# Kernel optimization log

Hardware: AMD Instinct MI355X
Metric: run time of the kernel (lower is better)

The kernel has to match this reference:

```python
import math
import jax, jax.numpy as jnp
import numpy as np

H = 12   # num attention heads
DH = 64  # head dim
K = 2    # pooling kernel
ST = 2   # pooling stride


def _alibi_slopes(n):
    def pow2_slopes(n):
        start = 2 ** (-2 ** (-(math.log2(n) - 3)))
        return [start * (start ** i) for i in range(n)]
    if math.log2(n).is_integer():
        return pow2_slopes(n)
    c = 2 ** math.floor(math.log2(n))
    return pow2_slopes(c) + _alibi_slopes(2 * c)[0::2][: n - c]


def _alibi_bias(p, s):
    # [1, H, p, s]; -slope * |i - j|
    rel = np.abs(np.arange(s)[None, :] - np.arange(p)[:, None]).astype(np.float32)
    slopes = np.asarray(_alibi_slopes(H), dtype=np.float32)
    return jnp.asarray((-slopes[:, None, None] * rel[None])[None])


def masked_avg_pool(x, mask):
    # x: [b, S, d] float, mask: [b, S] bool
    b, S, d = x.shape
    pad = (K - S) if K > S else (S - K) % ST
    if pad:
        x = jnp.pad(x, ((0, 0), (0, pad), (0, 0)))
        mask = jnp.pad(mask, ((0, 0), (0, pad)))
    p = (S + pad - K) // ST + 1
    idx = jnp.arange(p)[:, None] * ST + jnp.arange(K)[None, :]  # [p, K]
    xb = x[:, idx]        # [b, p, K, d]
    mb = mask[:, idx]     # [b, p, K]
    norm = jnp.maximum(mb.sum(-1), 1).astype(x.dtype)  # [b, p]
    y = (xb * mb[..., None].astype(x.dtype)).sum(-2) / norm[..., None]
    return y, mb.any(-1)


def setup_inputs() -> dict:
    key = jax.random.key(0)
    k1, k2, k3, k4 = jax.random.split(key, 4)
    B, S, D = 64, 512, 768
    return {
        "hidden_states": jax.random.normal(k1, (B, S, D), dtype=jnp.float32),
        "attention_mask": jax.random.randint(k2, (B, S), 0, 2, dtype=jnp.int32),
        "Wqkv_w": jax.random.normal(k3, (D, 3 * D), dtype=jnp.float32) * 0.02,
        "Wqkv_b": jax.random.normal(k4, (3 * D,), dtype=jnp.float32) * 0.02,
    }


def reference(hidden_states, attention_mask, Wqkv_w, Wqkv_b):
    mask = attention_mask.astype(bool)                    # [b, s]
    b, s, _ = hidden_states.shape
    # fused QKV proj; repad() zeroes padded rows
    qkv = (hidden_states @ Wqkv_w + Wqkv_b) * mask[..., None].astype(hidden_states.dtype)
    q, k, v = jnp.split(qkv, 3, axis=-1)                  # each [b, s, H*DH]
    # masked avg pooling of queries (flattened heads, as in the module)
    q_pooled, new_mask = masked_avg_pool(q, mask)         # [b, p, H*DH], [b, p]
    p = q_pooled.shape[1]
    qh = q_pooled.reshape(b, p, H, DH).transpose(0, 2, 1, 3)  # [b, H, p, DH]
    kh = k.reshape(b, s, H, DH).transpose(0, 2, 1, 3)         # [b, H, s, DH]
    vh = v.reshape(b, s, H, DH).transpose(0, 2, 1, 3)
    # additive bias: 0 where both query and key valid, else -10000; plus ALiBi
    pair = new_mask[:, :, None] & mask[:, None, :]            # [b, p, s]
    bias = jnp.where(pair, 0.0, -10000.0)[:, None] + _alibi_bias(p, s)  # [b, H, p, s]
    scores = jnp.einsum("bhpd,bhsd->bhps", qh, kh) / math.sqrt(DH) + bias
    attn = jax.nn.softmax(scores, axis=-1)
    out = jnp.einsum("bhps,bhsd->bhpd", attn, vh)             # [b, H, p, DH]
    attn_output = out.transpose(0, 2, 1, 3).reshape(b, p, H * DH)
    nm = new_mask[..., None].astype(attn_output.dtype)
    attn_output = attn_output * nm        # emulate unpad(): zero invalid rows
    residual_query = q_pooled * nm
    return attn_output, new_mask, residual_query
```

## Files before the change

### kernel.cpp

```cpp
#include <hip/hip_runtime.h>
#include <cstdint>
#include <cstddef>

#define HH 12
#define DHD 64
#define BB 64
#define SS 512
#define DD 768
#define PP 256
#define N3 2304

typedef __attribute__((ext_vector_type(8))) short bf16x8_t;
typedef __attribute__((ext_vector_type(4))) float f32x4_t;

__constant__ float c_slopes[12] = {
  0.5f, 0.25f, 0.125f, 0.0625f, 0.03125f, 0.015625f, 0.0078125f, 0.00390625f,
  0.70710678118654752f, 0.35355339059327376f, 0.17677669529663688f, 0.08838834764831844f
};

__device__ __forceinline__ ushort f2bf(float f) {
  union { float f; unsigned u; } v; v.f = f;
  unsigned r = v.u + 0x7fffu + ((v.u >> 16) & 1u);
  return (ushort)(r >> 16);
}
__device__ __forceinline__ float bf2f(ushort u) {
  union { unsigned u; float f; } v; v.u = ((unsigned)u) << 16;
  return v.f;
}
__device__ __forceinline__ void gload_lds16(const ushort* g, ushort* l) {
  __builtin_amdgcn_global_load_lds(
      (const __attribute__((address_space(1))) void*)g,
      (__attribute__((address_space(3))) void*)l, 16, 0, 0);
}

__global__ __launch_bounds__(256) void prep_kernel(const float* __restrict__ in,
                                                   ushort* __restrict__ out,
                                                   const float* __restrict__ W,
                                                   ushort* __restrict__ Wt) {
  if (blockIdx.x < 24576) {
    int i = blockIdx.x * 256 + threadIdx.x;
    float4 v = ((const float4*)in)[i];
    ushort4 o;
    o.x = f2bf(v.x); o.y = f2bf(v.y); o.z = f2bf(v.z); o.w = f2bf(v.w);
    ((ushort4*)out)[i] = o;
  } else {
    __shared__ float tile[32][33];
    int tb = blockIdx.x - 24576;
    int n0 = (tb % 72) * 32, k0 = (tb / 72) * 32;
    int tx = threadIdx.x & 31, ty = threadIdx.x >> 5;
    for (int r = ty; r < 32; r += 8) tile[r][tx] = W[(size_t)(k0 + r) * N3 + n0 + tx];
    __syncthreads();
    for (int r = ty; r < 32; r += 8) Wt[(size_t)(n0 + r) * DD + k0 + tx] = f2bf(tile[tx][r]);
  }
}

__global__ __launch_bounds__(512, 2) void gemm_qkv_kernel(
    const ushort* __restrict__ A, const ushort* __restrict__ Wt,
    const float* __restrict__ bias, const int* __restrict__ mask,
    ushort* __restrict__ qkv) {
  __shared__ __align__(16) ushort As[2][16384];
  __shared__ __align__(16) ushort Bs[2][16384];
  const int wg = blockIdx.x;
  const int swz = (wg & 7) * 144 + (wg >> 3);
  const int bm = (swz / 9) * 256;
  const int bn = (swz % 9) * 256;
  const int tid = threadIdx.x;
  const int lane = tid & 63;
  const int wave = tid >> 6;
  const int wm = (wave >> 2) * 128;
  const int wn = (wave & 3) * 64;
  const int fr = lane & 15, quad = lane >> 4;
  const int xr = (fr & 7) << 3;
  const int q8 = quad * 8;

  const int rsub = tid >> 3;
  const int cg8 = ((tid & 7) ^ (rsub & 7)) * 8;
  const ushort* Ag = A  + (size_t)(bm + rsub) * DD + cg8;
  const ushort* Bg = Wt + (size_t)(bn + rsub) * DD + cg8;
  ushort* AsW = &As[0][0] + wave * 512;
  ushort* BsW = &Bs[0][0] + wave * 512;

  f32x4_t acc[8][4];
#pragma unroll
  for (int i = 0; i < 8; i++)
#pragma unroll
    for (int j = 0; j < 4; j++) acc[i][j] = (f32x4_t){0.f, 0.f, 0.f, 0.f};

#pragma unroll
  for (int l = 0; l < 4; l++) {
    gload_lds16(Ag + (size_t)l * 64 * DD,      AsW + l * 4096);
    gload_lds16(Bg + (size_t)l * 64 * DD,      BsW + l * 4096);
  }
#pragma unroll
  for (int l = 0; l < 4; l++) {
    gload_lds16(Ag + (size_t)l * 64 * DD + 64, AsW + 16384 + l * 4096);
    gload_lds16(Bg + (size_t)l * 64 * DD + 64, BsW + 16384 + l * 4096);
  }
  asm volatile("s_waitcnt vmcnt(8)" ::: "memory");
  __builtin_amdgcn_s_barrier();
  asm volatile("" ::: "memory");

#pragma unroll 2
  for (int t = 0; t < 12; t++) {
    const ushort* Ab = &As[t & 1][0];
    const ushort* Bb = &Bs[t & 1][0];
    bf16x8_t a[4][2], b[4][2];
#pragma unroll
    for (int m = 0; m < 4; m++)
#pragma unroll
      for (int kk = 0; kk < 2; kk++)
        a[m][kk] = *(const bf16x8_t*)&Ab[(wm + m * 16 + fr) * 64 + ((kk * 32 + q8) ^ xr)];
#pragma unroll
    for (int n = 0; n < 4; n++)
#pragma unroll
      for (int kk = 0; kk < 2; kk++)
        b[n][kk] = *(const bf16x8_t*)&Bb[(wn + n * 16 + fr) * 64 + ((kk * 32 + q8) ^ xr)];
#pragma unroll
    for (int m = 0; m < 4; m++)
#pragma unroll
      for (int n = 0; n < 4; n++) {
        acc[m][n] = __builtin_amdgcn_mfma_f32_16x16x32_bf16(a[m][0], b[n][0], acc[m][n], 0, 0, 0);
        acc[m][n] = __builtin_amdgcn_mfma_f32_16x16x32_bf16(a[m][1], b[n][1], acc[m][n], 0, 0, 0);
      }
#pragma unroll
    for (int m = 0; m < 4; m++)
#pragma unroll
      for (int kk = 0; kk < 2; kk++)
        a[m][kk] = *(const bf16x8_t*)&Ab[(wm + 64 + m * 16 + fr) * 64 + ((kk * 32 + q8) ^ xr)];
#pragma unroll
    for (int m = 0; m < 4; m++)
#pragma unroll
      for (int n = 0; n < 4; n++) {
        acc[4 + m][n] = __builtin_amdgcn_mfma_f32_16x16x32_bf16(a[m][0], b[n][0], acc[4 + m][n], 0, 0, 0);
        acc[4 + m][n] = __builtin_amdgcn_mfma_f32_16x16x32_bf16(a[m][1], b[n][1], acc[4 + m][n], 0, 0, 0);
      }
    asm volatile("s_waitcnt lgkmcnt(0)" ::: "memory");
    __builtin_amdgcn_sched_barrier(0);
    __builtin_amdgcn_s_barrier();
    if (t < 10) {
      const size_t koff = (size_t)(t + 2) * 64;
      ushort* Ad = AsW + (t & 1) * 16384;
      ushort* Bd = BsW + (t & 1) * 16384;
#pragma unroll
      for (int l = 0; l < 4; l++) {
        gload_lds16(Ag + (size_t)l * 64 * DD + koff, Ad + l * 4096);
        gload_lds16(Bg + (size_t)l * 64 * DD + koff, Bd + l * 4096);
      }
      asm volatile("s_waitcnt vmcnt(8)" ::: "memory");
    } else {
      asm volatile("s_waitcnt vmcnt(0)" ::: "memory");
    }
    __builtin_amdgcn_s_barrier();
    asm volatile("" ::: "memory");
  }

  float bb[4];
#pragma unroll
  for (int j = 0; j < 4; j++) bb[j] = bias[bn + wn + j * 16 + fr];
#pragma unroll
  for (int i = 0; i < 8; i++) {
    const int gm = bm + wm + i * 16 + quad * 4;
#pragma unroll
    for (int r = 0; r < 4; r++) {
      const float mv = (float)mask[gm + r];
      ushort* orow = qkv + (size_t)(gm + r) * N3 + bn + wn + fr;
#pragma unroll
      for (int j = 0; j < 4; j++)
        orow[j * 16] = f2bf((acc[i][j][r] + bb[j]) * mv);
    }
  }
}

__global__ void pool_kernel(const ushort* __restrict__ qkv, const int* __restrict__ mask,
                            float* __restrict__ out, ushort* __restrict__ qp) {
  int idx = blockIdx.x * 256 + threadIdx.x;
  int d4 = idx % 192;
  int bp = idx / 192;
  int b = bp >> 8, p = bp & 255;
  int m0 = mask[b*512 + 2*p], m1 = mask[b*512 + 2*p + 1];
  int ms = m0 + m1;
  float inv = 1.0f / (float)(ms < 1 ? 1 : ms);
  const ushort* r0 = qkv + (size_t)(b*512 + 2*p) * N3 + d4*4;
  ushort4 x0 = *(const ushort4*)r0;
  ushort4 x1 = *(const ushort4*)(r0 + N3);
  float y0 = (bf2f(x0.x) + bf2f(x1.x)) * inv;
  float y1 = (bf2f(x0.y) + bf2f(x1.y)) * inv;
  float y2 = (bf2f(x0.z) + bf2f(x1.z)) * inv;
  float y3 = (bf2f(x0.w) + bf2f(x1.w)) * inv;
  float4 y = {y0, y1, y2, y3};
  *(float4*)(out + 12599296 + (size_t)bp * 768 + d4*4) = y;
  ushort4 q8;
  q8.x = f2bf(y0 * 0.125f); q8.y = f2bf(y1 * 0.125f);
  q8.z = f2bf(y2 * 0.125f); q8.w = f2bf(y3 * 0.125f);
  *(ushort4*)(qp + (size_t)bp * 768 + d4*4) = q8;
  if (d4 == 0) out[12582912 + bp] = (ms > 0) ? 1.0f : 0.0f;
}

__global__ __launch_bounds__(512, 2) void attn_kernel(
    const ushort* __restrict__ qkv, const ushort* __restrict__ qp,
    const int* __restrict__ mask, const float* __restrict__ nmask,
    float* __restrict__ outA) {
  __shared__ __align__(16) ushort K_lds[512 * 64];
  __shared__ __align__(16) ushort VT_lds[64 * 512];
  __shared__ __align__(16) ushort P_lds[8][32][40];
  __shared__ __align__(16) float  kb[512];
  const int h = blockIdx.x, b = blockIdx.y;
  const int tid = threadIdx.x, wave = tid >> 6, lane = tid & 63;
  const int fr = lane & 15, quad = lane >> 4;
  const int kxor = (fr & 7) << 4;
  const float slope = c_slopes[h];

  {
    const int r0 = lane >> 3;
    const int cg = ((lane & 7) ^ r0) * 8;
    const ushort* Ks = qkv + (size_t)(b * 512 + wave * 64 + r0) * N3 + 768 + h * 64 + cg;
#pragma unroll
    for (int i = 0; i < 8; i++)
      gload_lds16(Ks + (size_t)i * 8 * N3, K_lds + (wave * 64 + i * 8) * 64);
  }
  {
    const ushort* Vs = qkv + (size_t)(b * 512 + tid) * N3 + 1536 + h * 64;
    float4 vr[8];
#pragma unroll
    for (int d0 = 0; d0 < 8; d0++) vr[d0] = *(const float4*)(Vs + d0 * 8);
    const int s2 = tid * 2;
    const int sbase = (s2 & ~15), slo = (s2 & 15);
#pragma unroll
    for (int d0 = 0; d0 < 8; d0++) {
      ushort tmp[8];
      *(float4*)tmp = vr[d0];
#pragma unroll
      for (int j = 0; j < 8; j++) {
        int d = d0 * 8 + j;
        *(ushort*)((char*)VT_lds + (size_t)d * 1024 + ((sbase ^ ((d & 7) << 4)) + slo)) = tmp[j];
      }
    }
  }
  kb[tid] = mask[b * 512 + tid] ? 0.0f : -10000.0f;
  bf16x8_t qf[2][2];
#pragma unroll
  for (int nt = 0; nt < 2; nt++)
#pragma unroll
    for (int ks = 0; ks < 2; ks++)
      qf[nt][ks] = *(const bf16x8_t*)(qp + (size_t)(b * 256 + wave * 32 + nt * 16 + fr) * 768
                                      + h * 64 + ks * 32 + quad * 8);
  __syncthreads();

  const char* Kc = (const char*)K_lds;
  const char* Vc = (const char*)VT_lds;
  char* Pw = (char*)&P_lds[wave][0][0];

  f32x4_t O[2][4];
#pragma unroll
  for (int i = 0; i < 2; i++)
#pragma unroll
    for (int j = 0; j < 4; j++) O[i][j] = (f32x4_t){0.f, 0.f, 0.f, 0.f};
  float m_run[2] = {-3.0e38f, -3.0e38f};
  float l_run[2] = {0.f, 0.f};

  for (int sb = 0; sb < 512; sb += 64) {
    f32x4_t sacc[4][2];
#pragma unroll
    for (int mt = 0; mt < 4; mt++) { sacc[mt][0] = (f32x4_t){0,0,0,0}; sacc[mt][1] = (f32x4_t){0,0,0,0}; }
#pragma unroll
    for (int ks = 0; ks < 2; ks++)
#pragma unroll
      for (int mt = 0; mt < 4; mt++) {
        bf16x8_t ak = *(const bf16x8_t*)(Kc + (size_t)(sb + mt * 16 + fr) * 128
                                         + ((ks * 64 + quad * 16) ^ kxor));
        sacc[mt][0] = __builtin_amdgcn_mfma_f32_16x16x32_bf16(ak, qf[0][ks], sacc[mt][0], 0, 0, 0);
        sacc[mt][1] = __builtin_amdgcn_mfma_f32_16x16x32_bf16(ak, qf[1][ks], sacc[mt][1], 0, 0, 0);
      }
    float kbv[4][4];
#pragma unroll
    for (int mt = 0; mt < 4; mt++) {
      f32x4_t kv = *(const f32x4_t*)&kb[sb + mt * 16 + quad * 4];
#pragma unroll
      for (int r = 0; r < 4; r++) kbv[mt][r] = kv[r];
    }
    float pv2[2][4][4];
    float fsv[2];
#pragma unroll
    for (int nt = 0; nt < 2; nt++) {
      const float pidx = (float)(wave * 32 + nt * 16 + fr);
      float mx = -3.0e38f;
#pragma unroll
      for (int mt = 0; mt < 4; mt++)
#pragma unroll
        for (int r = 0; r < 4; r++) {
          float s_ = (float)(sb + mt * 16 + quad * 4 + r);
          float v = sacc[mt][nt][r] + kbv[mt][r] - slope * fabsf(s_ - pidx);
          pv2[nt][mt][r] = v;
          mx = fmaxf(mx, v);
        }
      mx = fmaxf(mx, __shfl_xor(mx, 16, 64));
      mx = fmaxf(mx, __shfl_xor(mx, 32, 64));
      float mnew = fmaxf(m_run[nt], mx);
      float f = __expf(m_run[nt] - mnew);
      m_run[nt] = mnew; fsv[nt] = f;
      float rs = 0.f;
#pragma unroll
      for (int mt = 0; mt < 4; mt++)
#pragma unroll
        for (int r = 0; r < 4; r++) {
          float e = __expf(pv2[nt][mt][r] - mnew);
          pv2[nt][mt][r] = e; rs += e;
        }
      rs += __shfl_xor(rs, 16, 64);
      rs += __shfl_xor(rs, 32, 64);
      l_run[nt] = l_run[nt] * f + rs;
    }
#pragma unroll
    for (int mp = 0; mp < 2; mp++)
#pragma unroll
      for (int r = 0; r < 4; r++) {
        float fb = __shfl(fsv[mp], quad * 4 + r, 64);
#pragma unroll
        for (int nd = 0; nd < 4; nd++) O[mp][nd][r] *= fb;
      }
#pragma unroll
    for (int c = 0; c < 2; c++) {
#pragma unroll
      for (int nt = 0; nt < 2; nt++)
#pragma unroll
        for (int mm = 0; mm < 2; mm++) {
          int mt = c * 2 + mm;
          ushort4 pk;
          pk.x = f2bf(pv2[nt][mt][0]); pk.y = f2bf(pv2[nt][mt][1]);
          pk.z = f2bf(pv2[nt][mt][2]); pk.w = f2bf(pv2[nt][mt][3]);
          *(ushort4*)(Pw + (nt * 16 + fr) * 80 + mm * 32 + quad * 8) = pk;
        }
      bf16x8_t ap0 = *(const bf16x8_t*)(Pw + fr * 80 + quad * 16);
      bf16x8_t ap1 = *(const bf16x8_t*)(Pw + (16 + fr) * 80 + quad * 16);
#pragma unroll
      for (int nd = 0; nd < 4; nd++) {
        bf16x8_t bv = *(const bf16x8_t*)(Vc + (size_t)(nd * 16 + fr) * 1024
                                         + (((sb + c * 32) * 2 + quad * 16) ^ kxor));
        O[0][nd] = __builtin_amdgcn_mfma_f32_16x16x32_bf16(ap0, bv, O[0][nd], 0, 0, 0);
        O[1][nd] = __builtin_amdgcn_mfma_f32_16x16x32_bf16(ap1, bv, O[1][nd], 0, 0, 0);
      }
    }
  }

#pragma unroll
  for (int mp = 0; mp < 2; mp++) {
    const int p0 = wave * 32 + mp * 16 + quad * 4;
#pragma unroll
    for (int r = 0; r < 4; r++) {
      float lb = __shfl(l_run[mp], quad * 4 + r, 64);
      float nm = nmask[b * 256 + p0 + r];
      float scl = nm / lb;
#pragma unroll
      for (int nd = 0; nd < 4; nd++)
        outA[(size_t)(b * 256 + p0 + r) * 768 + h * 64 + nd * 16 + fr] = O[mp][nd][r] * scl;
    }
  }
}

extern "C" void kernel_launch(void* const* d_in, const int* in_sizes, int n_in,
                              void* d_out, int out_size, void* d_ws, size_t ws_size,
                              hipStream_t stream) {
  const float* hs   = (const float*)d_in[0];
  const int*   mask = (const int*)d_in[1];
  const float* W    = (const float*)d_in[2];
  const float* bias = (const float*)d_in[3];
  float* out = (float*)d_out;
  char* ws = (char*)d_ws;
  ushort* A   = (ushort*)(ws);
  ushort* Wt  = (ushort*)(ws + 50331648);
  ushort* qkv = (ushort*)(ws + 53870592);
  ushort* qp  = (ushort*)(ws);

  hipLaunchKernelGGL(prep_kernel, dim3(26304), dim3(256), 0, stream, hs, A, W, Wt);
  hipLaunchKernelGGL(gemm_qkv_kernel, dim3(1152), dim3(512), 0, stream, A, Wt, bias, mask, qkv);
  hipLaunchKernelGGL(pool_kernel, dim3(12288), dim3(256), 0, stream, qkv, mask, out, qp);
  hipLaunchKernelGGL(attn_kernel, dim3(12, 64), dim3(512), 0, stream,
                     qkv, qp, mask, out + 12582912, out);
}
```

Before: 414.5 us.

## Pool hidden states before Q projection and drop separate pooling kernel

Because pooling is linear, the masked average of Q rows is computed by pooling the input hidden states first and then projecting, which halves the Q-projection GEMM work. The prep kernel now also writes the pooled bf16 inputs and the new mask. The GEMM epilogue writes K and V to separate compact buffers and emits the residual query and scaled bf16 Q directly, so the pool kernel and its read of the QKV intermediate go away. Applying the bias as bias*newmask matches the reference, which zeroes invalid rows before pooling. Pooling in fp32 before the bf16 cast slightly changes rounding compared with pooling bf16 Q values.

Result: faster. 389.8 us (-6.0%).

```diff
diff --git a/kernel.cpp b/kernel.cpp
--- a/kernel.cpp
+++ b/kernel.cpp
@@ -33,19 +33,48 @@
       (__attribute__((address_space(3))) void*)l, 16, 0, 0);
 }
 
-__global__ __launch_bounds__(256) void prep_kernel(const float* __restrict__ in,
-                                                   ushort* __restrict__ out,
-                                                   const float* __restrict__ W,
-                                                   ushort* __restrict__ Wt) {
-  if (blockIdx.x < 24576) {
-    int i = blockIdx.x * 256 + threadIdx.x;
-    float4 v = ((const float4*)in)[i];
-    ushort4 o;
-    o.x = f2bf(v.x); o.y = f2bf(v.y); o.z = f2bf(v.z); o.w = f2bf(v.w);
-    ((ushort4*)out)[i] = o;
+__global__ __launch_bounds__(256) void prep_kernel(
+    const float* __restrict__ hs, const int* __restrict__ mask,
+    ushort* __restrict__ A, ushort* __restrict__ Ap,
+    const float* __restrict__ W, ushort* __restrict__ Wt,
+    float* __restrict__ nmask_out) {
+  if (blockIdx.x < 8192) {
+    const int row0 = blockIdx.x * 4;
+    const int t = threadIdx.x;
+    if (t < 192) {
+      float4 v[4];
+#pragma unroll
+      for (int r = 0; r < 4; r++) {
+        v[r] = ((const float4*)hs)[(size_t)(row0 + r) * 192 + t];
+        ushort4 o;
+        o.x = f2bf(v[r].x); o.y = f2bf(v[r].y); o.z = f2bf(v[r].z); o.w = f2bf(v[r].w);
+        ((ushort4*)A)[(size_t)(row0 + r) * 192 + t] = o;
+      }
+      const int m0 = mask[row0], m1 = mask[row0 + 1];
+      const int m2 = mask[row0 + 2], m3 = mask[row0 + 3];
+      const float f0 = (float)m0, f1 = (float)m1, f2 = (float)m2, f3 = (float)m3;
+      const float inv0 = 1.0f / (float)((m0 + m1) < 1 ? 1 : (m0 + m1));
+      const float inv1 = 1.0f / (float)((m2 + m3) < 1 ? 1 : (m2 + m3));
+      ushort4 p0, p1;
+      p0.x = f2bf((f0 * v[0].x + f1 * v[1].x) * inv0);
+      p0.y = f2bf((f0 * v[0].y + f1 * v[1].y) * inv0);
+      p0.z = f2bf((f0 * v[0].z + f1 * v[1].z) * inv0);
+      p0.w = f2bf((f0 * v[0].w + f1 * v[1].w) * inv0);
+      p1.x = f2bf((f2 * v[2].x + f3 * v[3].x) * inv1);
+      p1.y = f2bf((f2 * v[2].y + f3 * v[3].y) * inv1);
+      p1.z = f2bf((f2 * v[2].z + f3 * v[3].z) * inv1);
+      p1.w = f2bf((f2 * v[2].w + f3 * v[3].w) * inv1);
+      const int prow = row0 >> 1;
+      ((ushort4*)Ap)[(size_t)prow * 192 + t]       = p0;
+      ((ushort4*)Ap)[(size_t)(prow + 1) * 192 + t] = p1;
+      if (t == 0) {
+        nmask_out[prow]     = (m0 + m1) > 0 ? 1.0f : 0.0f;
+        nmask_out[prow + 1] = (m2 + m3) > 0 ? 1.0f : 0.0f;
+      }
+    }
   } else {
     __shared__ float tile[32][33];
-    int tb = blockIdx.x - 24576;
+    int tb = blockIdx.x - 8192;
     int n0 = (tb % 72) * 32, k0 = (tb / 72) * 32;
     int tx = threadIdx.x & 31, ty = threadIdx.x >> 5;
     for (int r = ty; r < 32; r += 8) tile[r][tx] = W[(size_t)(k0 + r) * N3 + n0 + tx];
@@ -55,15 +84,18 @@
 }
 
 __global__ __launch_bounds__(512, 2) void gemm_qkv_kernel(
-    const ushort* __restrict__ A, const ushort* __restrict__ Wt,
-    const float* __restrict__ bias, const int* __restrict__ mask,
-    ushort* __restrict__ qkv) {
+    const ushort* __restrict__ A, const ushort* __restrict__ Ap,
+    const ushort* __restrict__ Wt, const float* __restrict__ bias,
+    const int* __restrict__ mask, const float* __restrict__ nmask,
+    ushort* __restrict__ Kbuf, ushort* __restrict__ Vbuf,
+    float* __restrict__ resid, ushort* __restrict__ qp) {
   __shared__ __align__(16) ushort As[2][16384];
   __shared__ __align__(16) ushort Bs[2][16384];
   const int wg = blockIdx.x;
-  const int swz = (wg & 7) * 144 + (wg >> 3);
-  const int bm = (swz / 9) * 256;
-  const int bn = (swz % 9) * 256;
+  const int swz = (wg & 7) * 120 + (wg >> 3);
+  int bm, wtb; const ushort* Asrc; bool isQ;
+  if (swz < 768) { isQ = false; bm = (swz / 6) * 256; wtb = 768 + (swz % 6) * 256; Asrc = A; }
+  else { isQ = true; int q = swz - 768; bm = (q / 3) * 256; wtb = (q % 3) * 256; Asrc = Ap; }
   const int tid = threadIdx.x;
   const int lane = tid & 63;
   const int wave = tid >> 6;
@@ -75,8 +107,8 @@
 
   const int rsub = tid >> 3;
   const int cg8 = ((tid & 7) ^ (rsub & 7)) * 8;
-  const ushort* Ag = A  + (size_t)(bm + rsub) * DD + cg8;
-  const ushort* Bg = Wt + (size_t)(bn + rsub) * DD + cg8;
+  const ushort* Ag = Asrc + (size_t)(bm + rsub) * DD + cg8;
+  const ushort* Bg = Wt + (size_t)(wtb + rsub) * DD + cg8;
   ushort* AsW = &As[0][0] + wave * 512;
   ushort* BsW = &Bs[0][0] + wave * 512;
 
@@ -156,48 +188,45 @@
 
   float bb[4];
 #pragma unroll
-  for (int j = 0; j < 4; j++) bb[j] = bias[bn + wn + j * 16 + fr];
-#pragma unroll
-  for (int i = 0; i < 8; i++) {
-    const int gm = bm + wm + i * 16 + quad * 4;
-#pragma unroll
-    for (int r = 0; r < 4; r++) {
-      const float mv = (float)mask[gm + r];
-      ushort* orow = qkv + (size_t)(gm + r) * N3 + bn + wn + fr;
-#pragma unroll
-      for (int j = 0; j < 4; j++)
-        orow[j * 16] = f2bf((acc[i][j][r] + bb[j]) * mv);
-    }
-  }
-}
-
-__global__ void pool_kernel(const ushort* __restrict__ qkv, const int* __restrict__ mask,
-                            float* __restrict__ out, ushort* __restrict__ qp) {
-  int idx = blockIdx.x * 256 + threadIdx.x;
-  int d4 = idx % 192;
-  int bp = idx / 192;
-  int b = bp >> 8, p = bp & 255;
-  int m0 = mask[b*512 + 2*p], m1 = mask[b*512 + 2*p + 1];
-  int ms = m0 + m1;
-  float inv = 1.0f / (float)(ms < 1 ? 1 : ms);
-  const ushort* r0 = qkv + (size_t)(b*512 + 2*p) * N3 + d4*4;
-  ushort4 x0 = *(const ushort4*)r0;
-  ushort4 x1 = *(const ushort4*)(r0 + N3);
-  float y0 = (bf2f(x0.x) + bf2f(x1.x)) * inv;
-  float y1 = (bf2f(x0.y) + bf2f(x1.y)) * inv;
-  float y2 = (bf2f(x0.z) + bf2f(x1.z)) * inv;
-  float y3 = (bf2f(x0.w) + bf2f(x1.w)) * inv;
-  float4 y = {y0, y1, y2, y3};
-  *(float4*)(out + 12599296 + (size_t)bp * 768 + d4*4) = y;
-  ushort4 q8;
-  q8.x = f2bf(y0 * 0.125f); q8.y = f2bf(y1 * 0.125f);
-  q8.z = f2bf(y2 * 0.125f); q8.w = f2bf(y3 * 0.125f);
-  *(ushort4*)(qp + (size_t)bp * 768 + d4*4) = q8;
-  if (d4 == 0) out[12582912 + bp] = (ms > 0) ? 1.0f : 0.0f;
+  for (int j = 0; j < 4; j++) bb[j] = bias[wtb + wn + j * 16 + fr];
+  if (!isQ) {
+    ushort* dst = (wtb < 1536) ? Kbuf : Vbuf;
+    const int cb = (wtb < 1536) ? (wtb - 768) : (wtb - 1536);
+#pragma unroll
+    for (int i = 0; i < 8; i++) {
+      const int gm = bm + wm + i * 16 + quad * 4;
+#pragma unroll
+      for (int r = 0; r < 4; r++) {
+        const float mv = (float)mask[gm + r];
+        ushort* orow = dst + (size_t)(gm + r) * DD + cb + wn + fr;
+#pragma unroll
+        for (int j = 0; j < 4; j++)
+          orow[j * 16] = f2bf((acc[i][j][r] + bb[j]) * mv);
+      }
+    }
+  } else {
+#pragma unroll
+    for (int i = 0; i < 8; i++) {
+      const int gm = bm + wm + i * 16 + quad * 4;
+#pragma unroll
+      for (int r = 0; r < 4; r++) {
+        const float qm = nmask[gm + r];
+        float* rrow = resid + (size_t)(gm + r) * DD + wtb + wn + fr;
+        ushort* qrow = qp + (size_t)(gm + r) * DD + wtb + wn + fr;
+#pragma unroll
+        for (int j = 0; j < 4; j++) {
+          float v = acc[i][j][r] + bb[j] * qm;
+          rrow[j * 16] = v;
+          qrow[j * 16] = f2bf(v * 0.125f);
+        }
+      }
+    }
+  }
 }
 
 __global__ __launch_bounds__(512, 2) void attn_kernel(
-    const ushort* __restrict__ qkv, const ushort* __restrict__ qp,
+    const ushort* __restrict__ Kbuf, const ushort* __restrict__ Vbuf,
+    const ushort* __restrict__ qp,
     const int* __restrict__ mask, const float* __restrict__ nmask,
     float* __restrict__ outA) {
   __shared__ __align__(16) ushort K_lds[512 * 64];
@@ -213,13 +242,13 @@
   {
     const int r0 = lane >> 3;
     const int cg = ((lane & 7) ^ r0) * 8;
-    const ushort* Ks = qkv + (size_t)(b * 512 + wave * 64 + r0) * N3 + 768 + h * 64 + cg;
+    const ushort* Ks = Kbuf + (size_t)(b * 512 + wave * 64 + r0) * DD + h * 64 + cg;
 #pragma unroll
     for (int i = 0; i < 8; i++)
-      gload_lds16(Ks + (size_t)i * 8 * N3, K_lds + (wave * 64 + i * 8) * 64);
+      gload_lds16(Ks + (size_t)i * 8 * DD, K_lds + (wave * 64 + i * 8) * 64);
   }
   {
-    const ushort* Vs = qkv + (size_t)(b * 512 + tid) * N3 + 1536 + h * 64;
+    const ushort* Vs = Vbuf + (size_t)(b * 512 + tid) * DD + h * 64;
     float4 vr[8];
 #pragma unroll
     for (int d0 = 0; d0 < 8; d0++) vr[d0] = *(const float4*)(Vs + d0 * 8);
@@ -366,14 +395,19 @@
   const float* bias = (const float*)d_in[3];
   float* out = (float*)d_out;
   char* ws = (char*)d_ws;
-  ushort* A   = (ushort*)(ws);
-  ushort* Wt  = (ushort*)(ws + 50331648);
-  ushort* qkv = (ushort*)(ws + 53870592);
-  ushort* qp  = (ushort*)(ws);
-
-  hipLaunchKernelGGL(prep_kernel, dim3(26304), dim3(256), 0, stream, hs, A, W, Wt);
-  hipLaunchKernelGGL(gemm_qkv_kernel, dim3(1152), dim3(512), 0, stream, A, Wt, bias, mask, qkv);
-  hipLaunchKernelGGL(pool_kernel, dim3(12288), dim3(256), 0, stream, qkv, mask, out, qp);
+  ushort* A    = (ushort*)(ws);
+  ushort* Wt   = (ushort*)(ws + 50331648);
+  ushort* Kbuf = (ushort*)(ws + 53870592);
+  ushort* Vbuf = (ushort*)(ws + 104202240);
+  ushort* Ap   = (ushort*)(ws + 154533888);
+  ushort* qp   = (ushort*)(ws + 179699712);
+  float* nmask = out + 12582912;
+  float* resid = out + 12599296;
+
+  hipLaunchKernelGGL(prep_kernel, dim3(9920), dim3(256), 0, stream,
+                     hs, mask, A, Ap, W, Wt, nmask);
+  hipLaunchKernelGGL(gemm_qkv_kernel, dim3(960), dim3(512), 0, stream,
+                     A, Ap, Wt, bias, mask, nmask, Kbuf, Vbuf, resid, qp);
   hipLaunchKernelGGL(attn_kernel, dim3(12, 64), dim3(512), 0, stream,
-                     qkv, qp, mask, out + 12582912, out);
-}
+                     Kbuf, Vbuf, qp, mask, nmask, out);
+}
```
